# Kernel optimization log

Measured on AMD Instinct MI355X. Metric: run time of the kernel, lower is better.

## Reference

```python
import jax, jax.numpy as jnp
import numpy as np

NEG_SLOPE = 0.2


def gat_layer(x, src, dst, W, attn_l, attn_r, bias):
    # x: [N, in_dim]; W: [in_dim, H*D]; attn_l/attn_r/bias: [H, D] / [H, D] / [H, D]
    N = x.shape[0]
    H, D = attn_l.shape
    feat = (x @ W).reshape(N, H, D)                      # [N, H, D]
    el = jnp.sum(feat * attn_l, axis=-1)                 # [N, H]
    er = jnp.sum(feat * attn_r, axis=-1)                 # [N, H]
    e = jax.nn.leaky_relu(el[src] + er[dst], NEG_SLOPE)  # [E, H]
    # edge softmax over incoming edges of each dst node (numerically stable)
    emax = jax.ops.segment_max(e, dst, num_segments=N)   # [N, H]
    ex = jnp.exp(e - emax[dst])                          # [E, H]
    denom = jax.ops.segment_sum(ex, dst, num_segments=N) # [N, H]
    alpha = ex / denom[dst]                              # [E, H]
    msg = alpha[:, :, None] * feat[src]                  # [E, H, D]
    rst = jax.ops.segment_sum(msg, dst, num_segments=N)  # [N, H, D]
    return rst + bias


def setup_inputs() -> dict:
    key = jax.random.key(0)
    ks = jax.random.split(key, 16)
    N, E = 50000, 800000
    IN, H, D, C = 128, 8, 16, 10
    HD = H * D  # 128
    s = lambda fan: 1.0 / np.sqrt(fan)
    return {
        "x": jax.random.normal(ks[0], (N, IN), jnp.float32),
        "src": jax.random.randint(ks[1], (E,), 0, N, jnp.int32),
        "dst": jax.random.randint(ks[2], (E,), 0, N, jnp.int32),
        "W1": jax.random.normal(ks[3], (IN, HD), jnp.float32) * s(IN),
        "al1": jax.random.normal(ks[4], (H, D), jnp.float32) * s(D),
        "ar1": jax.random.normal(ks[5], (H, D), jnp.float32) * s(D),
        "b1": jnp.zeros((H, D), jnp.float32),
        "W2": jax.random.normal(ks[6], (HD, HD), jnp.float32) * s(HD),
        "al2": jax.random.normal(ks[7], (H, D), jnp.float32) * s(D),
        "ar2": jax.random.normal(ks[8], (H, D), jnp.float32) * s(D),
        "b2": jnp.zeros((H, D), jnp.float32),
        "Wc": jax.random.normal(ks[9], (HD, C), jnp.float32) * s(HD),
        "bc": jnp.zeros((C,), jnp.float32),
    }


def reference(x, src, dst, W1, al1, ar1, b1, W2, al2, ar2, b2, Wc, bc):
    N = x.shape[0]
    h = gat_layer(x, src, dst, W1, al1, ar1, b1)       # [N, H, D]
    h = jax.nn.relu(h).reshape(N, -1)                  # [N, H*D]
    h = gat_layer(h, src, dst, W2, al2, ar2, b2)       # [N, H, D]
    hg = jnp.mean(h, axis=0).reshape(1, -1)            # mean_nodes, single graph -> [1, H*D]
    return hg @ Wc + bc                                # [1, num_classes]
```

## Files before the change

kernel.cpp:

```cpp
#include <hip/hip_runtime.h>
#include <hip/hip_bf16.h>

#define LEAKY 0.2f
#define BINB 8
#define TILE 4096
#define CAP 8192

static inline int ceil_div(int a, int b) { return (a + b - 1) / b; }

typedef __bf16 bf16x8 __attribute__((ext_vector_type(8)));
typedef float f32x4 __attribute__((ext_vector_type(4)));

__device__ __forceinline__ ushort f2bf(float f) {
    unsigned int x = __float_as_uint(f);
    unsigned int r = (x + 0x7fffu + ((x >> 16) & 1u)) >> 16;
    return (ushort)r;
}


__global__ __launch_bounds__(256) void bin_count(const int* __restrict__ dst,
                                                 int* __restrict__ bin_cnt, int E, int NB) {
    __shared__ int h[256];
    int t = threadIdx.x;
    h[t] = 0;
    __syncthreads();
    int base = blockIdx.x * TILE;
#pragma unroll
    for (int j = 0; j < TILE / 256; ++j) {
        int i = base + j * 256 + t;
        if (i < E) atomicAdd(&h[dst[i] >> BINB], 1);
    }
    __syncthreads();
    if (t < NB && h[t]) atomicAdd(&bin_cnt[t], h[t]);
}

__global__ __launch_bounds__(256) void bin_scan(const int* __restrict__ bin_cnt,
                                                int* __restrict__ binStart,
                                                int* __restrict__ bin_cursor,
                                                int* __restrict__ rowstart,
                                                int NB, int N, int E) {
    __shared__ int s[256];
    int t = threadIdx.x;
    int v = (t < NB) ? bin_cnt[t] : 0;
    s[t] = v;
    __syncthreads();
    for (int off = 1; off < 256; off <<= 1) {
        int x = (t >= off) ? s[t - off] : 0;
        __syncthreads();
        s[t] += x;
        __syncthreads();
    }
    int excl = s[t] - v;
    if (t < NB) {
        binStart[t] = excl;
        bin_cursor[t] = excl;
        if (t == NB - 1) binStart[NB] = excl + v;
    }
    if (t == 0) rowstart[N] = E;
}

__global__ __launch_bounds__(256) void bin_scatter(const int* __restrict__ src,
                                                   const int* __restrict__ dst,
                                                   int* __restrict__ bin_cursor,
                                                   unsigned int* __restrict__ coarse, int E) {
    __shared__ int hist[256], scn[256], gbase[256], lcur[256];
    __shared__ unsigned int outp[TILE];
    __shared__ int gidx[TILE];
    int t = threadIdx.x;
    hist[t] = 0;
    __syncthreads();
    int base = blockIdx.x * TILE;
    int dloc[TILE / 256];
#pragma unroll
    for (int j = 0; j < TILE / 256; ++j) {
        int i = base + j * 256 + t;
        int d = (i < E) ? dst[i] : -1;
        dloc[j] = d;
        if (d >= 0) atomicAdd(&hist[d >> BINB], 1);
    }
    __syncthreads();
    int hv = hist[t];
    scn[t] = hv;
    __syncthreads();
    for (int off = 1; off < 256; off <<= 1) {
        int x = (t >= off) ? scn[t - off] : 0;
        __syncthreads();
        scn[t] += x;
        __syncthreads();
    }
    int excl = scn[t] - hv;
    if (hv > 0) gbase[t] = atomicAdd(&bin_cursor[t], hv);
    lcur[t] = excl;
    scn[t] = excl;
    __syncthreads();
#pragma unroll
    for (int j = 0; j < TILE / 256; ++j) {
        int i = base + j * 256 + t;
        int d = dloc[j];
        if (d >= 0) {
            int b = d >> BINB;
            int pos = atomicAdd(&lcur[b], 1);
            outp[pos] = (unsigned int)src[i] | ((unsigned int)(d & ((1 << BINB) - 1)) << 16);
            gidx[pos] = gbase[b] + (pos - scn[b]);
        }
    }
    __syncthreads();
    int cnt = min(TILE, E - base);
    for (int j = t; j < cnt; j += 256) coarse[gidx[j]] = outp[j];
}

__global__ __launch_bounds__(256) void fine_csr(const unsigned int* __restrict__ coarse,
                                                const int* __restrict__ binStart,
                                                int* __restrict__ rowstart,
                                                ushort* __restrict__ bucket, int N) {
    __shared__ int hist[256], scn[256], cur[256];
    __shared__ ushort sb[CAP];
    int b = blockIdx.x, t = threadIdx.x;
    int e0 = binStart[b], e1 = binStart[b + 1];
    int cnt = e1 - e0;
    hist[t] = 0;
    __syncthreads();
    for (int j = e0 + t; j < e1; j += 256) atomicAdd(&hist[coarse[j] >> 16], 1);
    __syncthreads();
    int hv = hist[t];
    scn[t] = hv;
    __syncthreads();
    for (int off = 1; off < 256; off <<= 1) {
        int x = (t >= off) ? scn[t - off] : 0;
        __syncthreads();
        scn[t] += x;
        __syncthreads();
    }
    int excl = scn[t] - hv;
    int n = (b << BINB) + t;
    if (n < N) rowstart[n] = e0 + excl;
    cur[t] = excl;
    __syncthreads();
    bool fit = (cnt <= CAP);
    for (int j = e0 + t; j < e1; j += 256) {
        unsigned int p = coarse[j];
        int dl = p >> 16;
        int pos = atomicAdd(&cur[dl], 1);
        ushort sv = (ushort)(p & 0xffffu);
        if (fit) sb[pos] = sv;
        else bucket[e0 + pos] = sv;
    }
    __syncthreads();
    if (fit)
        for (int j = t; j < cnt; j += 256) bucket[e0 + j] = sb[j];
}

__global__ __launch_bounds__(256) void convert_w(const float* __restrict__ W1,
                                                 const float* __restrict__ W2,
                                                 ushort* __restrict__ Wt1,
                                                 ushort* __restrict__ Wt2) {
    int idx = blockIdx.x * 256 + threadIdx.x;
    const float* W = (idx < 16384) ? W1 : W2;
    ushort* O = (idx < 16384) ? Wt1 : Wt2;
    int i = idx & 16383;
    int k = i >> 7, n = i & 127;
    O[n * 128 + k] = f2bf(W[i]);
}

#define LDK 136
template <bool BF16IN>
__global__ __launch_bounds__(256) void gemm_attn_mfma(const void* __restrict__ in_,
                                                      const ushort* __restrict__ Wt,
                                                      const float* __restrict__ al,
                                                      const float* __restrict__ ar,
                                                      ushort* __restrict__ feat,
                                                      float* __restrict__ el,
                                                      float* __restrict__ er, int N) {
    __shared__ ushort sA[64 * LDK];
    int tid = threadIdx.x;
    int rowbase = blockIdx.x * 64;

    if (BF16IN) {
        const ushort* in = (const ushort*)in_;
#pragma unroll
        for (int i = 0; i < 4; ++i) {
            int idx8 = i * 256 + tid;
            int flat = idx8 * 8;
            int row = flat >> 7, col = flat & 127;
            int grow = rowbase + row;
            uint4 v = make_uint4(0, 0, 0, 0);
            if (grow < N) v = *reinterpret_cast<const uint4*>(in + (size_t)grow * 128 + col);
            *reinterpret_cast<uint4*>(&sA[row * LDK + col]) = v;
        }
    } else {
        const float* in = (const float*)in_;
#pragma unroll
        for (int i = 0; i < 8; ++i) {
            int idx4 = i * 256 + tid;
            int flat = idx4 * 4;
            int row = flat >> 7, col = flat & 127;
            int grow = rowbase + row;
            float4 v = make_float4(0.f, 0.f, 0.f, 0.f);
            if (grow < N) v = *reinterpret_cast<const float4*>(in + (size_t)grow * 128 + col);
            uint2 w;
            w.x = (unsigned int)f2bf(v.x) | ((unsigned int)f2bf(v.y) << 16);
            w.y = (unsigned int)f2bf(v.z) | ((unsigned int)f2bf(v.w) << 16);
            *reinterpret_cast<uint2*>(&sA[row * LDK + col]) = w;
        }
    }
    __syncthreads();

    int wid = tid >> 6;
    int lane = tid & 63;
    int wm = wid >> 1;
    int wn = wid & 1;
    int l15 = lane & 15;
    int lhi = lane >> 4;

    f32x4 acc[2][4] = {};
    const ushort* wb = Wt + (size_t)(wn * 64 + l15) * 128 + lhi * 8;
    const ushort* a0p = &sA[(wm * 32 + l15) * LDK + lhi * 8];
    const ushort* a1p = &sA[(wm * 32 + 16 + l15) * LDK + lhi * 8];

#pragma unroll
    for (int ks = 0; ks < 4; ++ks) {
        bf16x8 a0 = *reinterpret_cast<const bf16x8*>(a0p + ks * 32);
        bf16x8 a1 = *reinterpret_cast<const bf16x8*>(a1p + ks * 32);
#pragma unroll
        for (int ni = 0; ni < 4; ++ni) {
            bf16x8 b = *reinterpret_cast<const bf16x8*>(wb + ni * 16 * 128 + ks * 32);
            acc[0][ni] = __builtin_amdgcn_mfma_f32_16x16x32_bf16(a0, b, acc[0][ni], 0, 0, 0);
            acc[1][ni] = __builtin_amdgcn_mfma_f32_16x16x32_bf16(a1, b, acc[1][ni], 0, 0, 0);
        }
    }

#pragma unroll
    for (int ni = 0; ni < 4; ++ni) {
        int head = wn * 4 + ni;
        float alv = al[head * 16 + l15];
        float arv = ar[head * 16 + l15];
#pragma unroll
        for (int mi = 0; mi < 2; ++mi) {
#pragma unroll
            for (int reg = 0; reg < 4; ++reg) {
                int row = rowbase + wm * 32 + mi * 16 + lhi * 4 + reg;
                float v = acc[mi][ni][reg];
                float pl = v * alv;
                float pr = v * arv;
#pragma unroll
                for (int off = 8; off; off >>= 1) {
                    pl += __shfl_xor(pl, off);
                    pr += __shfl_xor(pr, off);
                }
                if (row < N) {
                    feat[(size_t)row * 128 + head * 16 + l15] = f2bf(v);
                    if (l15 == 0) {
                        el[row * 8 + head] = pl;
                        er[row * 8 + head] = pr;
                    }
                }
            }
        }
    }
}

__global__ __launch_bounds__(256) void aggregate(const ushort* __restrict__ feat,
                                                 const float* __restrict__ el,
                                                 const float* __restrict__ er,
                                                 const int* __restrict__ rowstart,
                                                 const ushort* __restrict__ bucket,
                                                 const float* __restrict__ bias,
                                                 ushort* __restrict__ out,
                                                 int N, int do_relu) {
    int wid = (blockIdx.x * 256 + threadIdx.x) >> 6;
    int lane = threadIdx.x & 63;
    if (wid >= N) return;
    int l7 = lane & 7;
    int e8 = lane >> 3;
    float erv = er[wid * 8 + l7];
    int beg = rowstart[wid];
    int end = rowstart[wid + 1];

    const unsigned int* fp = reinterpret_cast<const unsigned int*>(feat) + lane;

    float lsum = 0.0f, ax = 0.0f, ay = 0.0f;

    for (int base = beg; base < end; base += 64) {
        int cnt = min(end - base, 64);
        int myedge = base + lane;
        int sv64 = ((myedge < end) ? (int)bucket[myedge] : 0) << 6;

        int k = 0;
        for (; k + 8 <= cnt; k += 8) {
            int se = __shfl(sv64, k + e8);
            float e = el[(se >> 3) + l7] + erv;
            e = (e > 0.0f) ? e : LEAKY * e;
            float p = __expf(e);
            lsum += p;
#pragma unroll
            for (int q = 0; q < 8; ++q) {
                int su = __shfl(sv64, k + q);
                float pq = __shfl(p, q * 8 + e8);
                unsigned int u = fp[su];
                ax = fmaf(pq, __uint_as_float(u << 16), ax);
                ay = fmaf(pq, __uint_as_float(u & 0xffff0000u), ay);
            }
        }
        if (k < cnt) {
            int se = __shfl(sv64, min(k + e8, cnt - 1));
            bool valid = (k + e8) < cnt;
            float e = el[(se >> 3) + l7] + erv;
            e = (e > 0.0f) ? e : LEAKY * e;
            float p = valid ? __expf(e) : 0.0f;
            lsum += p;
#pragma unroll
            for (int q = 0; q < 8; ++q) {
                if (k + q < cnt) {
                    int su = __shfl(sv64, k + q);
                    float pq = __shfl(p, q * 8 + e8);
                    unsigned int u = fp[su];
                    ax = fmaf(pq, __uint_as_float(u << 16), ax);
                    ay = fmaf(pq, __uint_as_float(u & 0xffff0000u), ay);
                }
            }
        }
    }

    lsum += __shfl_xor(lsum, 8);
    lsum += __shfl_xor(lsum, 16);
    lsum += __shfl_xor(lsum, 32);
    float denom = __shfl(lsum, e8);
    float inv = (end > beg) ? 1.0f / denom : 0.0f;

    int c = lane * 2;
    float2 bv = *reinterpret_cast<const float2*>(bias + c);
    float ox = fmaf(ax, inv, bv.x);
    float oy = fmaf(ay, inv, bv.y);
    if (do_relu) {
        ox = fmaxf(ox, 0.0f);
        oy = fmaxf(oy, 0.0f);
    }
    unsigned int pk = (unsigned int)f2bf(ox) | ((unsigned int)f2bf(oy) << 16);
    reinterpret_cast<unsigned int*>(out)[(size_t)wid * 64 + lane] = pk;
}

__global__ __launch_bounds__(256) void mean_reduce(const ushort* __restrict__ h,
                                                   float* __restrict__ meanbuf, int N) {
    int c = threadIdx.x & 127;
    int rbase = blockIdx.x * 2 + (threadIdx.x >> 7);
    float s = 0.0f;
    for (int r = rbase; r < N; r += gridDim.x * 2)
        s += __uint_as_float((unsigned int)h[(size_t)r * 128 + c] << 16);
    atomicAdd(&meanbuf[c], s);
}

__global__ __launch_bounds__(64) void classifier(const float* __restrict__ meanbuf,
                                                 const float* __restrict__ Wc,
                                                 const float* __restrict__ bc,
                                                 float* __restrict__ outp, float invN) {
    int j = threadIdx.x;
    if (j < 10) {
        float s = 0.0f;
        for (int k = 0; k < 128; ++k) s += meanbuf[k] * invN * Wc[k * 10 + j];
        outp[j] = s + bc[j];
    }
}


extern "C" void kernel_launch(void* const* d_in, const int* in_sizes, int n_in,
                              void* d_out, int out_size, void* d_ws, size_t ws_size,
                              hipStream_t stream) {
    const float* x   = (const float*)d_in[0];
    const int*   src = (const int*)d_in[1];
    const int*   dst = (const int*)d_in[2];
    const float* W1  = (const float*)d_in[3];
    const float* al1 = (const float*)d_in[4];
    const float* ar1 = (const float*)d_in[5];
    const float* b1  = (const float*)d_in[6];
    const float* W2  = (const float*)d_in[7];
    const float* al2 = (const float*)d_in[8];
    const float* ar2 = (const float*)d_in[9];
    const float* b2  = (const float*)d_in[10];
    const float* Wc  = (const float*)d_in[11];
    const float* bc  = (const float*)d_in[12];

    int N = in_sizes[0] / 128;
    int E = in_sizes[1];
    int NB = (N + (1 << BINB) - 1) >> BINB;

    size_t off = 0;
    auto alloc = [&](size_t bytes) -> void* {
        void* p = (char*)d_ws + off;
        off += (bytes + 255) & ~size_t(255);
        return p;
    };
    int*   bin_cnt    = (int*)alloc(sizeof(int) * NB);
    int*   binStart   = (int*)alloc(sizeof(int) * (NB + 1));
    int*   bin_cursor = (int*)alloc(sizeof(int) * NB);
    int*   rowstart   = (int*)alloc(sizeof(int) * (N + 1));
    unsigned int* coarse = (unsigned int*)alloc(sizeof(unsigned int) * E);
    ushort* bucket  = (ushort*)alloc(sizeof(ushort) * E);
    ushort* feat    = (ushort*)alloc(sizeof(ushort) * (size_t)N * 128);
    float* el       = (float*)alloc(sizeof(float) * N * 8);
    float* er       = (float*)alloc(sizeof(float) * N * 8);
    ushort* h1      = (ushort*)alloc(sizeof(ushort) * (size_t)N * 128);
    ushort* h2      = (ushort*)alloc(sizeof(ushort) * (size_t)N * 128);
    float* meanbuf  = (float*)alloc(sizeof(float) * 128);
    ushort* Wt1     = (ushort*)alloc(sizeof(ushort) * 128 * 128);
    ushort* Wt2     = (ushort*)alloc(sizeof(ushort) * 128 * 128);

    hipMemsetAsync(bin_cnt, 0, sizeof(int) * NB, stream);
    hipMemsetAsync(meanbuf, 0, sizeof(float) * 128, stream);

    int GB = ceil_div(E, TILE);

    bin_count<<<GB, 256, 0, stream>>>(dst, bin_cnt, E, NB);
    bin_scan<<<1, 256, 0, stream>>>(bin_cnt, binStart, bin_cursor, rowstart, NB, N, E);
    bin_scatter<<<GB, 256, 0, stream>>>(src, dst, bin_cursor, coarse, E);
    fine_csr<<<NB, 256, 0, stream>>>(coarse, binStart, rowstart, bucket, N);
    convert_w<<<128, 256, 0, stream>>>(W1, W2, Wt1, Wt2);

    gemm_attn_mfma<false><<<ceil_div(N, 64), 256, 0, stream>>>(x, Wt1, al1, ar1, feat, el, er, N);
    aggregate<<<ceil_div(N * 64, 256), 256, 0, stream>>>(feat, el, er, rowstart, bucket, b1, h1, N, 1);
    gemm_attn_mfma<true><<<ceil_div(N, 64), 256, 0, stream>>>(h1, Wt2, al2, ar2, feat, el, er, N);
    aggregate<<<ceil_div(N * 64, 256), 256, 0, stream>>>(feat, el, er, rowstart, bucket, b2, h2, N, 0);
    mean_reduce<<<256, 256, 0, stream>>>(h2, meanbuf, N);
    classifier<<<1, 64, 0, stream>>>(meanbuf, Wc, bc, (float*)d_out, 1.0f / (float)N);
}
```

Before: 214.4 us.

## Stage edge attention weights in LDS instead of shuffles and halve binning tile

The aggregate kernel now walks edges in chunks of 8. Each lane computes one exp weight and writes it to a per-wave LDS array, and the weights are read back by head rather than broadcast through cross-lane shuffles. Source indices are reloaded from the bucket array per edge instead of being shuffled from a 64-edge register batch. The per-head softmax denominator is accumulated directly, which removes the final xor reduction. TILE is also halved from 4096 to 2048. The LDS staging has no barrier between write and read, so it relies on wave-synchronous execution, and the repeated bucket loads add memory traffic.

Result: slower. 241.9 us (median of 2 runs) (+12.8%).

```diff
diff --git a/kernel.cpp b/kernel.cpp
--- a/kernel.cpp
+++ b/kernel.cpp
@@ -3,7 +3,7 @@
 
 #define LEAKY 0.2f
 #define BINB 8
-#define TILE 4096
+#define TILE 2048
 #define CAP 8192
 
 static inline int ceil_div(int a, int b) { return (a + b - 1) / b; }
@@ -267,11 +267,14 @@
                                                  const float* __restrict__ bias,
                                                  ushort* __restrict__ out,
                                                  int N, int do_relu) {
+    __shared__ float pl[4][64];
+    int w = threadIdx.x >> 6;
     int wid = (blockIdx.x * 256 + threadIdx.x) >> 6;
     int lane = threadIdx.x & 63;
     if (wid >= N) return;
     int l7 = lane & 7;
     int e8 = lane >> 3;
+    int h = e8;
     float erv = er[wid * 8 + l7];
     int beg = rowstart[wid];
     int end = rowstart[wid + 1];
@@ -280,52 +283,39 @@
 
     float lsum = 0.0f, ax = 0.0f, ay = 0.0f;
 
-    for (int base = beg; base < end; base += 64) {
-        int cnt = min(end - base, 64);
-        int myedge = base + lane;
-        int sv64 = ((myedge < end) ? (int)bucket[myedge] : 0) << 6;
-
-        int k = 0;
-        for (; k + 8 <= cnt; k += 8) {
-            int se = __shfl(sv64, k + e8);
-            float e = el[(se >> 3) + l7] + erv;
-            e = (e > 0.0f) ? e : LEAKY * e;
-            float p = __expf(e);
-            lsum += p;
+    for (int base = beg; base < end; base += 8) {
+        int j1 = base + e8;
+        bool v1 = j1 < end;
+        int s1 = (int)bucket[v1 ? j1 : beg];
+        float e = el[s1 * 8 + l7] + erv;
+        e = (e > 0.0f) ? e : LEAKY * e;
+        float pv = v1 ? __expf(e) : 0.0f;
+        pl[w][lane] = pv;
+
+        int cnt = min(8, end - base);
+        if (cnt == 8) {
 #pragma unroll
             for (int q = 0; q < 8; ++q) {
-                int su = __shfl(sv64, k + q);
-                float pq = __shfl(p, q * 8 + e8);
-                unsigned int u = fp[su];
+                int s = (int)bucket[base + q];
+                float pq = pl[w][q * 8 + h];
+                unsigned int u = fp[s * 64];
+                lsum += pq;
                 ax = fmaf(pq, __uint_as_float(u << 16), ax);
                 ay = fmaf(pq, __uint_as_float(u & 0xffff0000u), ay);
             }
-        }
-        if (k < cnt) {
-            int se = __shfl(sv64, min(k + e8, cnt - 1));
-            bool valid = (k + e8) < cnt;
-            float e = el[(se >> 3) + l7] + erv;
-            e = (e > 0.0f) ? e : LEAKY * e;
-            float p = valid ? __expf(e) : 0.0f;
-            lsum += p;
-#pragma unroll
-            for (int q = 0; q < 8; ++q) {
-                if (k + q < cnt) {
-                    int su = __shfl(sv64, k + q);
-                    float pq = __shfl(p, q * 8 + e8);
-                    unsigned int u = fp[su];
-                    ax = fmaf(pq, __uint_as_float(u << 16), ax);
-                    ay = fmaf(pq, __uint_as_float(u & 0xffff0000u), ay);
-                }
+        } else {
+            for (int q = 0; q < cnt; ++q) {
+                int s = (int)bucket[base + q];
+                float pq = pl[w][q * 8 + h];
+                unsigned int u = fp[s * 64];
+                lsum += pq;
+                ax = fmaf(pq, __uint_as_float(u << 16), ax);
+                ay = fmaf(pq, __uint_as_float(u & 0xffff0000u), ay);
             }
         }
     }
 
-    lsum += __shfl_xor(lsum, 8);
-    lsum += __shfl_xor(lsum, 16);
-    lsum += __shfl_xor(lsum, 32);
-    float denom = __shfl(lsum, e8);
-    float inv = (end > beg) ? 1.0f / denom : 0.0f;
+    float inv = (end > beg) ? 1.0f / lsum : 0.0f;
 
     int c = lane * 2;
     float2 bv = *reinterpret_cast<const float2*>(bias + c);
```
